# Optimization experiments

Hardware: AMD Instinct MI355X
Metric: run time of the kernel (lower is better)

Reference implementation:

```python
import jax, jax.numpy as jnp
import numpy as np

N, F, H, K = 8192, 128, 128, 16
E = N * 32


def _mlp(f, w1, b1, w2, b2, w3, b3):
    h = jax.nn.relu(f @ w1 + b1)
    h = jax.nn.relu(h @ w2 + b2)
    return h @ w3 + b3


def _edge_conv(x, w1, b1, w2, b2, w3, b3, k):
    # dynamic kNN in feature space (includes self like torch_cluster.knn with x==y)
    sn = jnp.sum(x * x, axis=1)
    d = sn[:, None] + sn[None, :] - 2.0 * (x @ x.T)  # [N,N] squared dists
    idx = jax.lax.top_k(-d, k)[1]                    # [N,k] nearest neighbors
    xj = x[idx]                                      # [N,k,H]
    xi = jnp.broadcast_to(x[:, None, :], xj.shape)
    f = jnp.concatenate([xi, xj - xi], axis=-1)      # [N,k,2H]
    return jnp.max(_mlp(f, w1, b1, w2, b2, w3, b3), axis=1)  # max aggregation


def _gcn(x, w, b, src, dst, norm, n):
    h = x @ w
    out = jax.ops.segment_sum(norm[:, None] * h[src], dst, num_segments=n)
    return out + b


def _forward(x, edge_index, edge_weight,
             wg1, bg1, wg2, bg2, wg3, bg3,
             e1w1, e1b1, e1w2, e1b2, e1w3, e1b3,
             e2w1, e2b1, e2w2, e2b2, e2w3, e2b3,
             e3w1, e3b1, e3w2, e3b2, e3w3, e3b3):
    n = x.shape[0]
    loop = jnp.arange(n)
    src = jnp.concatenate([edge_index[0], loop])  # source j
    dst = jnp.concatenate([edge_index[1], loop])  # target i
    ew = jnp.concatenate([edge_weight, jnp.ones((n,), x.dtype)])  # self-loop weight 1
    deg = jax.ops.segment_sum(ew, dst, num_segments=n)
    dis = jnp.where(deg > 0, jax.lax.rsqrt(jnp.maximum(deg, 1e-12)), 0.0)
    norm = dis[src] * ew * dis[dst]

    n1 = jnp.tanh(_gcn(x, wg1, bg1, src, dst, norm, n))   # dropout is identity at eval
    e1 = _edge_conv(n1, e1w1, e1b1, e1w2, e1b2, e1w3, e1b3, K)
    e1_n1 = jnp.linalg.norm(e1 + n1, axis=1, keepdims=True)  # [N,1]

    n2 = jnp.tanh(_gcn(n1, wg2, bg2, src, dst, norm, n))
    e2 = _edge_conv(n2, e2w1, e2b1, e2w2, e2b2, e2w3, e2b3, K)
    e2_n2 = e2 + n2

    n3 = jnp.tanh(_gcn(n2, wg3, bg3, src, dst, norm, n))
    e3 = _edge_conv(n3, e3w1, e3b1, e3w2, e3b2, e3w3, e3b3, K)
    e3_n3 = e3 + n3

    x2 = e1_n1 * e2_n2 * e3_n3
    return jax.nn.log_softmax(x2, axis=1)


def setup_inputs() -> dict:
    key = jax.random.key(0)
    ks = jax.random.split(key, 32)
    inp = {
        'x': jax.random.normal(ks[0], (N, F), dtype=jnp.float32),
        'edge_index': jax.random.randint(ks[1], (2, E), 0, N, dtype=jnp.int64) if jax.config.jax_enable_x64 else jax.random.randint(ks[1], (2, E), 0, N).astype(jnp.int32),
        'edge_weight': jax.random.uniform(ks[2], (E,), dtype=jnp.float32),
    }
    s = 0.05
    gcn_in = [F, H, H]
    for i in range(3):
        inp[f'wg{i+1}'] = jax.random.normal(ks[3 + i], (gcn_in[i], H), dtype=jnp.float32) * s
        inp[f'bg{i+1}'] = jnp.zeros((H,), jnp.float32)
    dims = [(2 * H, 64), (64, H), (H, H)]
    kk = 6
    for c in range(1, 4):
        for j, (di, do) in enumerate(dims):
            inp[f'e{c}w{j+1}'] = jax.random.normal(ks[kk], (di, do), dtype=jnp.float32) * s
            inp[f'e{c}b{j+1}'] = jnp.zeros((do,), jnp.float32)
            kk += 1
    return inp


def reference(x, edge_index, edge_weight,
              wg1, bg1, wg2, bg2, wg3, bg3,
              e1w1, e1b1, e1w2, e1b2, e1w3, e1b3,
              e2w1, e2b1, e2w2, e2b2, e2w3, e2b3,
              e3w1, e3b1, e3w2, e3b2, e3w3, e3b3):
    return _forward(x, edge_index, edge_weight,
                    wg1, bg1, wg2, bg2, wg3, bg3,
                    e1w1, e1b1, e1w2, e1b2, e1w3, e1b3,
                    e2w1, e2b1, e2w2, e2b2, e2w3, e2b3,
                    e3w1, e3b1, e3w2, e3b2, e3w3, e3b3)
```

## Files before the change

### kernel.cpp

```cpp
#include <hip/hip_runtime.h>
#include <math.h>

#define N_ 8192
#define H_ 128
#define E_ 262144
#define K_ 16
#define SLABJ 1024
#define CHUNKJ 512

typedef __attribute__((ext_vector_type(8))) short bshort8;
typedef __attribute__((ext_vector_type(16))) float f32x16;
typedef unsigned long long u64;

__global__ void k_deg_init(float* deg) {
  int i = blockIdx.x * 256 + threadIdx.x;
  deg[i] = 1.0f;
}

__global__ void k_deg_scatter(const int* __restrict__ ei, const float* __restrict__ ew,
                              float* deg) {
  int e = blockIdx.x * 256 + threadIdx.x;
  atomicAdd(&deg[ei[E_ + e]], ew[e]);
}

__global__ void k_dis(float* deg) {
  int i = blockIdx.x * 256 + threadIdx.x;
  deg[i] = rsqrtf(deg[i]);
}

__global__ void k_hist(const int* __restrict__ ei, int* hist) {
  int e = blockIdx.x * 256 + threadIdx.x;
  atomicAdd(&hist[ei[E_ + e]], 1);
}

__global__ void k_scan(int* hist, int* rowptr) {
  __shared__ int part[256];
  __shared__ int partx[257];
  int t = threadIdx.x;
  int base = t * 32;
  int loc[32];
  int s = 0;
#pragma unroll
  for (int i = 0; i < 32; ++i) { loc[i] = s; s += hist[base + i]; }
  part[t] = s;
  __syncthreads();
  if (t == 0) {
    int r = 0;
    for (int i = 0; i < 256; ++i) { partx[i] = r; r += part[i]; }
    partx[256] = r;
  }
  __syncthreads();
  int b = partx[t];
#pragma unroll
  for (int i = 0; i < 32; ++i) {
    rowptr[base + i] = b + loc[i];
    hist[base + i] = b + loc[i];
  }
  if (t == 0) rowptr[N_] = partx[256];
}

__global__ void k_edgebuild(const int* __restrict__ ei, const float* __restrict__ ew,
                            const float* __restrict__ dis, int* cursor,
                            int* __restrict__ srcS, float* __restrict__ normS) {
  int e = blockIdx.x * 256 + threadIdx.x;
  int s = ei[e], d = ei[E_ + e];
  int pos = atomicAdd(&cursor[d], 1);
  srcS[pos] = s;
  normS[pos] = dis[s] * ew[e] * dis[d];
}

__device__ __forceinline__ unsigned short f2bf_rne(float x) {
  unsigned u = __builtin_bit_cast(unsigned, x);
  unsigned r = ((u >> 16) & 1u) + 0x7fffu;
  return (unsigned short)((u + r) >> 16);
}
__device__ __forceinline__ float bf2f(unsigned short b) {
  unsigned u = ((unsigned)b) << 16;
  return __builtin_bit_cast(float, u);
}

struct WP { const float* p[12]; };

__global__ void k_wprepAll(WP wp, bshort8* __restrict__ wAll) {
  int id = blockIdx.x * 256 + threadIdx.x;
  int layer = id / 7168;
  int r = id - layer * 7168;
  bshort8* base = wAll + layer * 14336;
  const float* src;
  bshort8 *dH, *dL;
  int slot, kind;
  if (r < 2048)      { kind = 0; slot = r;        src = wp.p[layer*4+0]; dH = base;         dL = base + 2048; }
  else if (r < 4096) { kind = 1; slot = r - 2048; src = wp.p[layer*4+1]; dH = base + 4096;  dL = base + 6144; }
  else if (r < 5120) { kind = 2; slot = r - 4096; src = wp.p[layer*4+2]; dH = base + 8192;  dL = base + 9216; }
  else               { kind = 3; slot = r - 5120; src = wp.p[layer*4+3]; dH = base + 10240; dL = base + 12288; }
  int lane = slot & 63;
  int n, k0;
  if (kind == 2) {
    int ks = (slot >> 6) & 3, nt = slot >> 8;
    n = nt * 32 + (lane & 31);
    k0 = ks * 16 + (lane >> 5) * 8;
  } else {
    int ks = (slot >> 6) & 7, nt = slot >> 9;
    n = nt * 32 + (lane & 31);
    k0 = ks * 16 + (lane >> 5) * 8;
  }
  bshort8 h, l;
#pragma unroll
  for (int i = 0; i < 8; ++i) {
    int k = k0 + i;
    float v;
    if (kind == 1) v = (n < 64) ? (src[k * 64 + n] - src[(128 + k) * 64 + n])
                                : src[(128 + k) * 64 + (n - 64)];
    else v = src[k * 128 + n];
    unsigned short hb = f2bf_rne(v);
    h[i] = (short)hb;
    l[i] = (short)f2bf_rne(v - bf2f(hb));
  }
  dH[slot] = h;
  dL[slot] = l;
}

__global__ __launch_bounds__(256, 3) void k_gemmM(const float* __restrict__ A,
                                                  const bshort8* __restrict__ wfH,
                                                  const bshort8* __restrict__ wfL,
                                                  float* __restrict__ C) {
  __shared__ short aHs[32 * 132], aLs[32 * 132];
  int t = threadIdx.x;
  int r0 = blockIdx.x * 32;
  int w = t >> 6, lane = t & 63, q = lane & 31, half = lane >> 5;

  {
    int r = t >> 3;
    int kc = (t & 7) * 16;
    const float* p = A + (r0 + r) * 128 + kc;
#pragma unroll
    for (int e4 = 0; e4 < 4; ++e4) {
      float4 v = *(const float4*)(p + e4 * 4);
      float vals[4] = {v.x, v.y, v.z, v.w};
      unsigned short hs[4], ls[4];
#pragma unroll
      for (int i = 0; i < 4; ++i) {
        hs[i] = f2bf_rne(vals[i]);
        ls[i] = f2bf_rne(vals[i] - bf2f(hs[i]));
      }
      int off = r * 132 + kc + e4 * 4;
      *(u64*)&aHs[off] = ((u64)hs[0]) | ((u64)hs[1] << 16) | ((u64)hs[2] << 32) | ((u64)hs[3] << 48);
      *(u64*)&aLs[off] = ((u64)ls[0]) | ((u64)ls[1] << 16) | ((u64)ls[2] << 32) | ((u64)ls[3] << 48);
    }
  }
  bshort8 bH[8], bL[8];
#pragma unroll
  for (int ks = 0; ks < 8; ++ks) {
    bH[ks] = wfH[(w * 8 + ks) * 64 + lane];
    bL[ks] = wfL[(w * 8 + ks) * 64 + lane];
  }
  __syncthreads();

  f32x16 accP, accQ;
#pragma unroll
  for (int r = 0; r < 16; ++r) { accP[r] = 0.f; accQ[r] = 0.f; }
#pragma unroll
  for (int ks = 0; ks < 8; ++ks) {
    int off = q * 132 + ks * 16 + half * 8;
    union { bshort8 v; u64 u[2]; } aH, aL;
    aH.u[0] = *(const u64*)&aHs[off];
    aH.u[1] = *(const u64*)&aHs[off + 4];
    aL.u[0] = *(const u64*)&aLs[off];
    aL.u[1] = *(const u64*)&aLs[off + 4];
    accQ = __builtin_amdgcn_mfma_f32_32x32x16_bf16(aL.v, bH[ks], accQ, 0, 0, 0);
    accQ = __builtin_amdgcn_mfma_f32_32x32x16_bf16(aH.v, bL[ks], accQ, 0, 0, 0);
    accP = __builtin_amdgcn_mfma_f32_32x32x16_bf16(aH.v, bH[ks], accP, 0, 0, 0);
  }
#pragma unroll
  for (int reg = 0; reg < 16; ++reg) {
    int row = (reg & 3) + 8 * (reg >> 2) + 4 * half;
    C[(r0 + row) * 128 + w * 32 + q] = accP[reg] + accQ[reg];
  }
}

__global__ void k_gemmMF(const bshort8* __restrict__ fAH, const bshort8* __restrict__ fAL,
                         const bshort8* __restrict__ wfH, const bshort8* __restrict__ wfL,
                         float* __restrict__ C) {
  int t = threadIdx.x;
  int rt = blockIdx.x >> 1;
  int w = (blockIdx.x & 1) * 2 + (t >> 6);
  int lane = t & 63, q = lane & 31, half = lane >> 5;

  bshort8 bH[8], bL[8], aH[8], aL[8];
#pragma unroll
  for (int ks = 0; ks < 8; ++ks) {
    bH[ks] = wfH[(w * 8 + ks) * 64 + lane];
    bL[ks] = wfL[(w * 8 + ks) * 64 + lane];
    aH[ks] = fAH[(rt * 8 + ks) * 64 + lane];
    aL[ks] = fAL[(rt * 8 + ks) * 64 + lane];
  }
  f32x16 accP, accQ;
#pragma unroll
  for (int r = 0; r < 16; ++r) { accP[r] = 0.f; accQ[r] = 0.f; }
#pragma unroll
  for (int ks = 0; ks < 8; ++ks) {
    accQ = __builtin_amdgcn_mfma_f32_32x32x16_bf16(aL[ks], bH[ks], accQ, 0, 0, 0);
    accQ = __builtin_amdgcn_mfma_f32_32x32x16_bf16(aH[ks], bL[ks], accQ, 0, 0, 0);
    accP = __builtin_amdgcn_mfma_f32_32x32x16_bf16(aH[ks], bH[ks], accP, 0, 0, 0);
  }
#pragma unroll
  for (int reg = 0; reg < 16; ++reg) {
    int row = (reg & 3) + 8 * (reg >> 2) + 4 * half;
    C[(rt * 32 + row) * 128 + w * 32 + q] = accP[reg] + accQ[reg];
  }
}

__global__ __launch_bounds__(256) void k_gcn_agg(const float* __restrict__ h,
                                                 const float* __restrict__ dis,
                                                 const int* __restrict__ rowptr,
                                                 const int* __restrict__ srcS,
                                                 const float* __restrict__ normS,
                                                 const float* __restrict__ bg,
                                                 float* __restrict__ n_out,
                                                 float* __restrict__ sn) {
  __shared__ float part[4];
  int t = threadIdx.x;
  int i = blockIdx.x * 2 + (t >> 7);
  int c = t & 127;
  float di = dis[i];
  float a0 = di * di * h[i * 128 + c], a1 = 0.f, a2 = 0.f, a3 = 0.f;
  int e0 = rowptr[i], e1 = rowptr[i + 1];
  int e = e0;
  for (; e + 4 <= e1; e += 4) {
    int s0 = srcS[e], s1 = srcS[e + 1], s2 = srcS[e + 2], s3 = srcS[e + 3];
    float w0 = normS[e], w1 = normS[e + 1], w2 = normS[e + 2], w3 = normS[e + 3];
    a0 += w0 * h[s0 * 128 + c];
    a1 += w1 * h[s1 * 128 + c];
    a2 += w2 * h[s2 * 128 + c];
    a3 += w3 * h[s3 * 128 + c];
  }
  for (; e < e1; ++e) a0 += normS[e] * h[srcS[e] * 128 + c];
  float v = tanhf(a0 + a1 + a2 + a3 + bg[c]);
  n_out[i * 128 + c] = v;
  float vv = v * v;
#pragma unroll
  for (int off = 32; off; off >>= 1) vv += __shfl_down(vv, off, 64);
  if ((t & 63) == 0) part[t >> 6] = vv;
  __syncthreads();
  if ((t & 127) == 0) sn[i] = part[t >> 6] + part[(t >> 6) + 1];
}

__global__ void k_fragprep(const float* __restrict__ src, bshort8* __restrict__ hiA,
                           bshort8* __restrict__ loA) {
  int t = blockIdx.x * 256 + threadIdx.x;
  int j = t >> 4, slot = t & 15;
  const float* p = src + j * 128 + slot * 8;
  float4 f0 = *(const float4*)p;
  float4 f1 = *(const float4*)(p + 4);
  float f[8] = {f0.x, f0.y, f0.z, f0.w, f1.x, f1.y, f1.z, f1.w};
  bshort8 h, l;
#pragma unroll
  for (int i = 0; i < 8; ++i) {
    unsigned short hb = f2bf_rne(f[i]);
    h[i] = (short)hb;
    l[i] = (short)f2bf_rne(f[i] - bf2f(hb));
  }
  int ks = slot >> 1, half = slot & 1;
  int dst = ((j >> 5) * 8 + ks) * 64 + half * 32 + (j & 31);
  hiA[dst] = h;
  loA[dst] = l;
}

__device__ __forceinline__ u64 packkey(float d, int j) {
  unsigned m = __builtin_bit_cast(unsigned, d);
  m = (m & 0x80000000u) ? ~m : (m | 0x80000000u);
  return (((u64)m) << 32) | (unsigned)j;
}

__device__ __forceinline__ float unpackd(u64 key) {
  unsigned m = (unsigned)(key >> 32);
  unsigned u = (m & 0x80000000u) ? (m & 0x7fffffffu) : ~m;
  return __builtin_bit_cast(float, u);
}

__device__ __forceinline__ void ins4(u64* tk, u64 x) {
  bool c[4];
#pragma unroll
  for (int s = 0; s < 4; ++s) c[s] = x < tk[s];
#pragma unroll
  for (int s = 3; s >= 1; --s) tk[s] = c[s - 1] ? tk[s - 1] : (c[s] ? x : tk[s]);
  tk[0] = c[0] ? x : tk[0];
}

__device__ __forceinline__ void ins16(u64* tk, u64 x) {
  bool c[16];
#pragma unroll
  for (int s = 0; s < 16; ++s) c[s] = x < tk[s];
#pragma unroll
  for (int s = 15; s >= 1; --s) tk[s] = c[s - 1] ? tk[s - 1] : (c[s] ? x : tk[s]);
  tk[0] = c[0] ? x : tk[0];
}

__global__ __launch_bounds__(256, 2) void k_knnA(const bshort8* __restrict__ fragHi,
                                                 const bshort8* __restrict__ fragLo,
                                                 const float* __restrict__ sn,
                                                 u64* __restrict__ candR) {
  __shared__ float snS[CHUNKJ];
  int t = threadIdx.x;
  int qtile = blockIdx.x, chunk = blockIdx.y;
  int wave = t >> 6, lane = t & 63;
  int q = lane & 31, half = lane >> 5;

  snS[t] = sn[chunk * CHUNKJ + t];
  snS[t + 256] = sn[chunk * CHUNKJ + t + 256];

  bshort8 bHi[8], bLo[8];
#pragma unroll
  for (int ks = 0; ks < 8; ++ks) {
    int o = (qtile * 8 + ks) * 64 + lane;
    bHi[ks] = fragHi[o];
    bLo[ks] = fragLo[o];
  }
  __syncthreads();

  u64 tk[4];
#pragma unroll
  for (int s = 0; s < 4; ++s) tk[s] = ~0ULL;

  int jt0 = chunk * 16 + wave * 4;
  bshort8 pH[4], pL[4];
#pragma unroll
  for (int k4 = 0; k4 < 4; ++k4) {
    int o = (jt0 * 8 + k4) * 64 + lane;
    pH[k4] = fragHi[o];
    pL[k4] = fragLo[o];
  }

  for (int ti = 0; ti < 4; ++ti) {
    int jt = jt0 + ti;
    f32x16 accP, accQ;
#pragma unroll
    for (int r = 0; r < 16; ++r) { accP[r] = 0.f; accQ[r] = 0.f; }

    bshort8 qH[4], qL[4];
#pragma unroll
    for (int k4 = 0; k4 < 4; ++k4) {
      int o = (jt * 8 + 4 + k4) * 64 + lane;
      qH[k4] = fragHi[o];
      qL[k4] = fragLo[o];
    }
#pragma unroll
    for (int k4 = 0; k4 < 4; ++k4) {
      accQ = __builtin_amdgcn_mfma_f32_32x32x16_bf16(pL[k4], bHi[k4], accQ, 0, 0, 0);
      accQ = __builtin_amdgcn_mfma_f32_32x32x16_bf16(pH[k4], bLo[k4], accQ, 0, 0, 0);
      accP = __builtin_amdgcn_mfma_f32_32x32x16_bf16(pH[k4], bHi[k4], accP, 0, 0, 0);
    }
    if (ti < 3) {
#pragma unroll
      for (int k4 = 0; k4 < 4; ++k4) {
        int o = ((jt + 1) * 8 + k4) * 64 + lane;
        pH[k4] = fragHi[o];
        pL[k4] = fragLo[o];
      }
    }
#pragma unroll
    for (int k4 = 0; k4 < 4; ++k4) {
      accQ = __builtin_amdgcn_mfma_f32_32x32x16_bf16(qL[k4], bHi[4 + k4], accQ, 0, 0, 0);
      accQ = __builtin_amdgcn_mfma_f32_32x32x16_bf16(qH[k4], bLo[4 + k4], accQ, 0, 0, 0);
      accP = __builtin_amdgcn_mfma_f32_32x32x16_bf16(qH[k4], bHi[4 + k4], accP, 0, 0, 0);
    }

    int jbase = (wave * 4 + ti) * 32;
#pragma unroll
    for (int rp = 0; rp < 8; ++rp) {
      int r0 = rp * 2;
      int row0 = (r0 & 3) + 8 * (r0 >> 2) + 4 * half;
      float d0 = snS[jbase + row0] - 2.0f * (accP[r0] + accQ[r0]);
      float d1 = snS[jbase + row0 + 1] - 2.0f * (accP[r0 + 1] + accQ[r0 + 1]);
      u64 k0 = packkey(d0, chunk * CHUNKJ + jbase + row0);
      u64 k1 = packkey(d1, chunk * CHUNKJ + jbase + row0 + 1);
      u64 km = k0 < k1 ? k0 : k1;
      if (km < tk[3]) {
        if (k0 < tk[3]) ins4(tk, k0);
        if (k1 < tk[3]) ins4(tk, k1);
      }
    }
  }

  int g = wave * 2 + half;
#pragma unroll
  for (int s = 0; s < 4; ++s)
    candR[(size_t)(chunk * 32 + g * 4 + s) * N_ + qtile * 32 + q] = tk[s];
}

__global__ __launch_bounds__(256) void k_tauseedX(const u64* __restrict__ candR,
                                                  int* __restrict__ cursor,
                                                  float* __restrict__ tauD) {
  __shared__ u64 mb[64 * 65];
  int t = threadIdx.x;
  int ql = t >> 2, j = t & 3;
  int q = blockIdx.x * 64 + ql;

  int rb[8];
#pragma unroll
  for (int k = 0; k < 8; ++k) {
    int L = 8 * j + k;
    rb[k] = (L >> 3) * 32 + (L & 7) * 4;
  }
  int h0 = 0, h1 = 0, h2 = 0, h3 = 0, h4 = 0, h5 = 0, h6 = 0, h7 = 0;
  for (int step = 0; step < 16; ++step) {
    u64 best = (h0 < 4) ? candR[(size_t)(rb[0] + h0) * N_ + q] : ~0ULL;
    int bg = 0;
    u64 b;
    b = (h1 < 4) ? candR[(size_t)(rb[1] + h1) * N_ + q] : ~0ULL; if (b < best) { best = b; bg = 1; }
    b = (h2 < 4) ? candR[(size_t)(rb[2] + h2) * N_ + q] : ~0ULL; if (b < best) { best = b; bg = 2; }
    b = (h3 < 4) ? candR[(size_t)(rb[3] + h3) * N_ + q] : ~0ULL; if (b < best) { best = b; bg = 3; }
    b = (h4 < 4) ? candR[(size_t)(rb[4] + h4) * N_ + q] : ~0ULL; if (b < best) { best = b; bg = 4; }
    b = (h5 < 4) ? candR[(size_t)(rb[5] + h5) * N_ + q] : ~0ULL; if (b < best) { best = b; bg = 5; }
    b = (h6 < 4) ? candR[(size_t)(rb[6] + h6) * N_ + q] : ~0ULL; if (b < best) { best = b; bg = 6; }
    b = (h7 < 4) ? candR[(size_t)(rb[7] + h7) * N_ + q] : ~0ULL; if (b < best) { best = b; bg = 7; }
    mb[ql * 65 + j * 16 + step] = best;
    h0 += (bg == 0); h1 += (bg == 1); h2 += (bg == 2); h3 += (bg == 3);
    h4 += (bg == 4); h5 += (bg == 5); h6 += (bg == 6); h7 += (bg == 7);
  }
  __syncthreads();
  if (t < 64) {
    int qq = blockIdx.x * 64 + t;
    int base = t * 65;
    int g0 = 0, g1 = 0, g2 = 0, g3 = 0;
    u64 best = 0;
    for (int step = 0; step < 16; ++step) {
      best = mb[base + g0];
      int bg = 0;
      u64 b;
      b = mb[base + 16 + g1]; if (b < best) { best = b; bg = 1; }
      b = mb[base + 32 + g2]; if (b < best) { best = b; bg = 2; }
      b = mb[base + 48 + g3]; if (b < best) { best = b; bg = 3; }
      g0 += (bg == 0); g1 += (bg == 1); g2 += (bg == 2); g3 += (bg == 3);
    }
    tauD[qq] = unpackd(best);
    cursor[qq] = 0;
  }
}

__global__ __launch_bounds__(256, 2) void k_knnB(const bshort8* __restrict__ fragHi,
                                                 const bshort8* __restrict__ fragLo,
                                                 const float* __restrict__ sn,
                                                 const float* __restrict__ tauD,
                                                 int* __restrict__ cursor,
                                                 u64* __restrict__ accept,
                                                 u64* __restrict__ accExt) {
  __shared__ float snS[SLABJ];
  int t = threadIdx.x;
  int qtile = blockIdx.x, slab = blockIdx.y;
  int wave = t >> 6, lane = t & 63;
  int q = lane & 31, half = lane >> 5;
  int qg = qtile * 32 + q;

#pragma unroll
  for (int p = 0; p < 4; ++p) snS[t + 256 * p] = sn[slab * SLABJ + t + 256 * p];

  bshort8 bHi[8], bLo[8];
#pragma unroll
  for (int ks = 0; ks < 8; ++ks) {
    int o = (qtile * 8 + ks) * 64 + lane;
    bHi[ks] = fragHi[o];
    bLo[ks] = fragLo[o];
  }
  float tD = tauD[qg];
  __syncthreads();

  u64 buf[6];
  int cnt = 0;

  int jt0 = slab * 32 + wave * 8;
  bshort8 pH[4], pL[4];
#pragma unroll
  for (int k4 = 0; k4 < 4; ++k4) {
    int o = (jt0 * 8 + k4) * 64 + lane;
    pH[k4] = fragHi[o];
    pL[k4] = fragLo[o];
  }

  for (int ti = 0; ti < 8; ++ti) {
    int jt = jt0 + ti;
    f32x16 accP, accQ;
#pragma unroll
    for (int r = 0; r < 16; ++r) { accP[r] = 0.f; accQ[r] = 0.f; }

    bshort8 qH[4], qL[4];
#pragma unroll
    for (int k4 = 0; k4 < 4; ++k4) {
      int o = (jt * 8 + 4 + k4) * 64 + lane;
      qH[k4] = fragHi[o];
      qL[k4] = fragLo[o];
    }
#pragma unroll
    for (int k4 = 0; k4 < 4; ++k4) {
      accQ = __builtin_amdgcn_mfma_f32_32x32x16_bf16(pL[k4], bHi[k4], accQ, 0, 0, 0);
      accQ = __builtin_amdgcn_mfma_f32_32x32x16_bf16(pH[k4], bLo[k4], accQ, 0, 0, 0);
      accP = __builtin_amdgcn_mfma_f32_32x32x16_bf16(pH[k4], bHi[k4], accP, 0, 0, 0);
    }
    if (ti < 7) {
#pragma unroll
      for (int k4 = 0; k4 < 4; ++k4) {
        int o = ((jt + 1) * 8 + k4) * 64 + lane;
        pH[k4] = fragHi[o];
        pL[k4] = fragLo[o];
      }
    }
#pragma unroll
    for (int k4 = 0; k4 < 4; ++k4) {
      accQ = __builtin_amdgcn_mfma_f32_32x32x16_bf16(qL[k4], bHi[4 + k4], accQ, 0, 0, 0);
      accQ = __builtin_amdgcn_mfma_f32_32x32x16_bf16(qH[k4], bLo[4 + k4], accQ, 0, 0, 0);
      accP = __builtin_amdgcn_mfma_f32_32x32x16_bf16(qH[k4], bHi[4 + k4], accP, 0, 0, 0);
    }

    int jbase = (wave * 8 + ti) * 32;
#pragma unroll
    for (int rp = 0; rp < 8; ++rp) {
      int r0 = rp * 2;
      int row0 = (r0 & 3) + 8 * (r0 >> 2) + 4 * half;
      float d0 = snS[jbase + row0] - 2.0f * (accP[r0] + accQ[r0]);
      float d1 = snS[jbase + row0 + 1] - 2.0f * (accP[r0 + 1] + accQ[r0 + 1]);
      if (d0 <= tD) {
        u64 k0 = packkey(d0, slab * SLABJ + jbase + row0);
        if (cnt < 6) {
#pragma unroll
          for (int s = 0; s < 6; ++s)
            if (s == cnt) buf[s] = k0;
          ++cnt;
        } else {
          int pos = atomicAdd(&cursor[qg], 1);
          if (pos < 128) accept[(size_t)pos * N_ + qg] = k0;
          else if (pos < 192) accExt[(size_t)(pos - 128) * N_ + qg] = k0;
        }
      }
      if (d1 <= tD) {
        u64 k1 = packkey(d1, slab * SLABJ + jbase + row0 + 1);
        if (cnt < 6) {
#pragma unroll
          for (int s = 0; s < 6; ++s)
            if (s == cnt) buf[s] = k1;
          ++cnt;
        } else {
          int pos = atomicAdd(&cursor[qg], 1);
          if (pos < 128) accept[(size_t)pos * N_ + qg] = k1;
          else if (pos < 192) accExt[(size_t)(pos - 128) * N_ + qg] = k1;
        }
      }
    }
  }

  if (cnt > 0) {
    int pos = atomicAdd(&cursor[qg], cnt);
#pragma unroll
    for (int s = 0; s < 6; ++s) {
      if (s < cnt) {
        int slot = pos + s;
        if (slot < 128) accept[(size_t)slot * N_ + qg] = buf[s];
        else if (slot < 192) accExt[(size_t)(slot - 128) * N_ + qg] = buf[s];
      }
    }
  }
}

__global__ __launch_bounds__(256) void k_select(const u64* __restrict__ accept,
                                                const u64* __restrict__ accExt,
                                                const int* __restrict__ cursor,
                                                int* __restrict__ idxo) {
  __shared__ u64 mb[64 * 65];
  int t = threadIdx.x;
  int ql = t >> 2;
  int j = t & 3;
  int q = blockIdx.x * 64 + ql;
  int c = cursor[q];
  if (c > 192) c = 192;
  u64 tk[16];
#pragma unroll
  for (int s = 0; s < 16; ++s) tk[s] = ~0ULL;
  for (int i = j; i < c; i += 4) {
    u64 x = (i < 128) ? accept[(size_t)i * N_ + q] : accExt[(size_t)(i - 128) * N_ + q];
    if (x < tk[15]) ins16(tk, x);
  }
#pragma unroll
  for (int s = 0; s < 16; ++s) mb[ql * 65 + j * 16 + s] = tk[s];
  __syncthreads();
  if (t < 64) {
    int qq = blockIdx.x * 64 + t;
    int base = t * 65;
    int h0 = 0, h1 = 0, h2 = 0, h3 = 0;
    for (int step = 0; step < 16; ++step) {
      u64 best = mb[base + h0];
      int bg = 0;
      u64 b;
      b = mb[base + 16 + h1]; if (b < best) { best = b; bg = 1; }
      b = mb[base + 32 + h2]; if (b < best) { best = b; bg = 2; }
      b = mb[base + 48 + h3]; if (b < best) { best = b; bg = 3; }
      idxo[qq * 16 + step] = (int)(unsigned)(best & 0xffffffffULL);
      h0 += (bg == 0); h1 += (bg == 1); h2 += (bg == 2); h3 += (bg == 3);
    }
  }
}

__global__ __launch_bounds__(256, 3) void k_mlpM(
    const float* __restrict__ ab, const int* __restrict__ idx,
    const bshort8* __restrict__ w2fH, const bshort8* __restrict__ w2fL,
    const bshort8* __restrict__ w3fH, const bshort8* __restrict__ w3fL,
    const float* __restrict__ b1g, const float* __restrict__ b2g,
    const float* __restrict__ b3g, const float* __restrict__ nadd,
    float* __restrict__ eout) {
  __shared__ short h1H[64 * 68], h1L[64 * 68];
  __shared__ short h2H[64 * 132], h2L[64 * 132];
  int t = threadIdx.x;
  int n0 = blockIdx.x * 4;
  int w = t >> 6, lane = t & 63, q = lane & 31, half = lane >> 5;

  {
    int r = t >> 2;
    int kc = (t & 3) * 16;
    int node = n0 + (r >> 4);
    int jn = idx[node * 16 + (r & 15)];
    const float* pa = ab + node * 128 + kc;
    const float* pb = ab + jn * 128 + 64 + kc;
    const float* p1 = b1g + kc;
#pragma unroll
    for (int e4 = 0; e4 < 4; ++e4) {
      float4 va = *(const float4*)(pa + e4 * 4);
      float4 vb = *(const float4*)(pb + e4 * 4);
      float4 v1 = *(const float4*)(p1 + e4 * 4);
      float vals[4] = {va.x + vb.x + v1.x, va.y + vb.y + v1.y,
                       va.z + vb.z + v1.z, va.w + vb.w + v1.w};
      unsigned short hs[4], ls[4];
#pragma unroll
      for (int i = 0; i < 4; ++i) {
        float v = fmaxf(vals[i], 0.f);
        hs[i] = f2bf_rne(v);
        ls[i] = f2bf_rne(v - bf2f(hs[i]));
      }
      int off = r * 68 + kc + e4 * 4;
      *(u64*)&h1H[off] = ((u64)hs[0]) | ((u64)hs[1] << 16) | ((u64)hs[2] << 32) | ((u64)hs[3] << 48);
      *(u64*)&h1L[off] = ((u64)ls[0]) | ((u64)ls[1] << 16) | ((u64)ls[2] << 32) | ((u64)ls[3] << 48);
    }
  }

  bshort8 c2H[4], c2L[4];
#pragma unroll
  for (int ks = 0; ks < 4; ++ks) {
    c2H[ks] = w2fH[(w * 4 + ks) * 64 + lane];
    c2L[ks] = w2fL[(w * 4 + ks) * 64 + lane];
  }
  bshort8 c3H[8], c3L[8];
#pragma unroll
  for (int ks = 0; ks < 8; ++ks) {
    c3H[ks] = w3fH[(w * 8 + ks) * 64 + lane];
    c3L[ks] = w3fL[(w * 8 + ks) * 64 + lane];
  }
  float bias2 = b2g[w * 32 + q];
  float bias3 = b3g[w * 32 + q];
  __syncthreads();

#pragma unroll
  for (int rt = 0; rt < 2; ++rt) {
    f32x16 acc;
#pragma unroll
    for (int r = 0; r < 16; ++r) acc[r] = 0.f;
#pragma unroll
    for (int ks = 0; ks < 4; ++ks) {
      int off = (rt * 32 + q) * 68 + ks * 16 + half * 8;
      union { bshort8 v; u64 u[2]; } aH, aL;
      aH.u[0] = *(const u64*)&h1H[off];
      aH.u[1] = *(const u64*)&h1H[off + 4];
      aL.u[0] = *(const u64*)&h1L[off];
      aL.u[1] = *(const u64*)&h1L[off + 4];
      acc = __builtin_amdgcn_mfma_f32_32x32x16_bf16(aL.v, c2H[ks], acc, 0, 0, 0);
      acc = __builtin_amdgcn_mfma_f32_32x32x16_bf16(aH.v, c2L[ks], acc, 0, 0, 0);
      acc = __builtin_amdgcn_mfma_f32_32x32x16_bf16(aH.v, c2H[ks], acc, 0, 0, 0);
    }
#pragma unroll
    for (int reg = 0; reg < 16; ++reg) {
      int row = rt * 32 + (reg & 3) + 8 * (reg >> 2) + 4 * half;
      float v = fmaxf(acc[reg] + bias2, 0.f);
      unsigned short hb = f2bf_rne(v);
      h2H[row * 132 + w * 32 + q] = (short)hb;
      h2L[row * 132 + w * 32 + q] = (short)f2bf_rne(v - bf2f(hb));
    }
  }
  __syncthreads();

#pragma unroll
  for (int rt = 0; rt < 2; ++rt) {
    f32x16 acc;
#pragma unroll
    for (int r = 0; r < 16; ++r) acc[r] = 0.f;
#pragma unroll
    for (int ks = 0; ks < 8; ++ks) {
      int off = (rt * 32 + q) * 132 + ks * 16 + half * 8;
      union { bshort8 v; u64 u[2]; } aH, aL;
      aH.u[0] = *(const u64*)&h2H[off];
      aH.u[1] = *(const u64*)&h2H[off + 4];
      aL.u[0] = *(const u64*)&h2L[off];
      aL.u[1] = *(const u64*)&h2L[off + 4];
      acc = __builtin_amdgcn_mfma_f32_32x32x16_bf16(aL.v, c3H[ks], acc, 0, 0, 0);
      acc = __builtin_amdgcn_mfma_f32_32x32x16_bf16(aH.v, c3L[ks], acc, 0, 0, 0);
      acc = __builtin_amdgcn_mfma_f32_32x32x16_bf16(aH.v, c3H[ks], acc, 0, 0, 0);
    }
    float mA = -INFINITY, mB = -INFINITY;
#pragma unroll
    for (int reg = 0; reg < 8; ++reg) mA = fmaxf(mA, acc[reg]);
#pragma unroll
    for (int reg = 8; reg < 16; ++reg) mB = fmaxf(mB, acc[reg]);
    mA = fmaxf(mA, __shfl_xor(mA, 32, 64));
    mB = fmaxf(mB, __shfl_xor(mB, 32, 64));
    int col = w * 32 + q;
    int nodeA = n0 + rt * 2, nodeB = n0 + rt * 2 + 1;
    if (half == 0) {
      float v = mA + bias3;
      if (nadd) v += nadd[nodeA * 128 + col];
      eout[nodeA * 128 + col] = v;
    } else {
      float v = mB + bias3;
      if (nadd) v += nadd[nodeB * 128 + col];
      eout[nodeB * 128 + col] = v;
    }
  }
}

__global__ void k_e1n1(const float* __restrict__ e1, const float* __restrict__ n1,
                       float* s1) {
  int t = threadIdx.x;
  int node = blockIdx.x * 4 + (t >> 6);
  int lane = t & 63;
  float v0 = e1[node * 128 + lane] + n1[node * 128 + lane];
  float v1 = e1[node * 128 + 64 + lane] + n1[node * 128 + 64 + lane];
  float ss = v0 * v0 + v1 * v1;
#pragma unroll
  for (int off = 32; off; off >>= 1) ss += __shfl_down(ss, off, 64);
  if (lane == 0) s1[node] = sqrtf(ss);
}

__global__ void k_final(const float* __restrict__ s1, const float* __restrict__ e2n2,
                        const float* __restrict__ e3n3, float* __restrict__ out) {
  int t = threadIdx.x;
  int node = blockIdx.x * 4 + (t >> 6);
  int lane = t & 63;
  float s = s1[node];
  float z0 = s * e2n2[node * 128 + lane] * e3n3[node * 128 + lane];
  float z1 = s * e2n2[node * 128 + 64 + lane] * e3n3[node * 128 + 64 + lane];
  float m = fmaxf(z0, z1);
#pragma unroll
  for (int off = 32; off; off >>= 1) m = fmaxf(m, __shfl_xor(m, off, 64));
  float ex = expf(z0 - m) + expf(z1 - m);
#pragma unroll
  for (int off = 32; off; off >>= 1) ex += __shfl_xor(ex, off, 64);
  float lse = m + logf(ex);
  out[node * 128 + lane] = z0 - lse;
  out[node * 128 + 64 + lane] = z1 - lse;
}

extern "C" void kernel_launch(void* const* d_in, const int* in_sizes, int n_in,
                              void* d_out, int out_size, void* d_ws, size_t ws_size,
                              hipStream_t stream) {
  (void)in_sizes; (void)n_in; (void)out_size;
  const float* x  = (const float*)d_in[0];
  const int* ei   = (const int*)d_in[1];
  const float* ew = (const float*)d_in[2];
  const float* wg[3] = {(const float*)d_in[3], (const float*)d_in[5], (const float*)d_in[7]};
  const float* bg[3] = {(const float*)d_in[4], (const float*)d_in[6], (const float*)d_in[8]};
  const float* ew1[3] = {(const float*)d_in[9],  (const float*)d_in[15], (const float*)d_in[21]};
  const float* eb1[3] = {(const float*)d_in[10], (const float*)d_in[16], (const float*)d_in[22]};
  const float* ew2[3] = {(const float*)d_in[11], (const float*)d_in[17], (const float*)d_in[23]};
  const float* eb2[3] = {(const float*)d_in[12], (const float*)d_in[18], (const float*)d_in[24]};
  const float* ew3[3] = {(const float*)d_in[13], (const float*)d_in[19], (const float*)d_in[25]};
  const float* eb3[3] = {(const float*)d_in[14], (const float*)d_in[20], (const float*)d_in[26]};

  size_t small = (size_t)(23 * N_ + (N_ + 256) + N_ + 2 * E_);
  size_t need = (small + 172032 + (size_t)7 * N_ * H_) * sizeof(float);
  if (ws_size < need) return;

  float* ws  = (float*)d_ws;
  float* dis = ws;
  float* sn  = ws + N_;
  float* S1  = ws + 2 * N_;
  int* idx   = (int*)(ws + 3 * N_);
  int* cursor = (int*)(ws + 21 * N_);
  float* tauD = ws + 22 * N_;
  int* rowptr = (int*)(ws + 23 * N_);
  int* hist   = rowptr + N_ + 256;
  int* srcS   = hist + N_;
  float* normS = (float*)(srcS + E_);
  bshort8* wAll = (bshort8*)(normS + E_);
  float* h   = (float*)(normS + E_ + 172032);
  float* n1  = h + N_ * H_;
  float* n2  = n1 + N_ * H_;
  float* n3  = n2 + N_ * H_;
  float* E2  = n3 + N_ * H_;
  float* E1  = E2 + N_ * H_;
  float* ab  = E1 + N_ * H_;

  bshort8* fragHi = (bshort8*)h;
  bshort8* fragLo = (bshort8*)(h + N_ * H_ / 2);
  u64* candR  = (u64*)E1;
  u64* accept = (u64*)E1;

  float* nl[3] = {n1, n2, n3};
  float* spare[3] = {n2, n1, n2};
  float* nadd[3] = {nullptr, n2, n3};

  k_deg_init<<<N_ / 256, 256, 0, stream>>>(dis);
  k_deg_scatter<<<E_ / 256, 256, 0, stream>>>(ei, ew, dis);
  k_dis<<<N_ / 256, 256, 0, stream>>>(dis);
  hipMemsetAsync(hist, 0, N_ * sizeof(int), stream);
  k_hist<<<E_ / 256, 256, 0, stream>>>(ei, hist);
  k_scan<<<1, 256, 0, stream>>>(hist, rowptr);
  k_edgebuild<<<E_ / 256, 256, 0, stream>>>(ei, ew, dis, hist, srcS, normS);

  WP wp;
  for (int l = 0; l < 3; ++l) {
    wp.p[l * 4 + 0] = wg[l];
    wp.p[l * 4 + 1] = ew1[l];
    wp.p[l * 4 + 2] = ew2[l];
    wp.p[l * 4 + 3] = ew3[l];
  }
  k_wprepAll<<<84, 256, 0, stream>>>(wp, wAll);

  for (int l = 0; l < 3; ++l) {
    bshort8* wl = wAll + l * 14336;
    bshort8* wgfH = wl;            bshort8* wgfL = wl + 2048;
    bshort8* w1fH = wl + 4096;     bshort8* w1fL = wl + 6144;
    bshort8* w2fH = wl + 8192;     bshort8* w2fL = wl + 9216;
    bshort8* w3fH = wl + 10240;    bshort8* w3fL = wl + 12288;

    const float* inp = (l == 0) ? x : nl[l - 1];
    k_gemmM<<<256, 256, 0, stream>>>(inp, wgfH, wgfL, h);
    k_gcn_agg<<<N_ / 2, 256, 0, stream>>>(h, dis, rowptr, srcS, normS, bg[l], nl[l], sn);
    k_fragprep<<<N_ * 16 / 256, 256, 0, stream>>>(nl[l], fragHi, fragLo);
    k_knnA<<<dim3(N_ / 32, 4), 256, 0, stream>>>(fragHi, fragLo, sn, candR);
    k_tauseedX<<<N_ / 64, 256, 0, stream>>>(candR, cursor, tauD);
    k_knnB<<<dim3(N_ / 32, 8), 256, 0, stream>>>(fragHi, fragLo, sn, tauD, cursor,
                                                 accept, (u64*)spare[l]);
    k_select<<<N_ / 64, 256, 0, stream>>>(accept, (u64*)spare[l], cursor, idx);
    k_gemmMF<<<512, 128, 0, stream>>>(fragHi, fragLo, w1fH, w1fL, ab);
    float* etgt = (l == 1) ? E2 : E1;
    k_mlpM<<<N_ / 4, 256, 0, stream>>>(ab, idx, w2fH, w2fL, w3fH, w3fL,
                                       eb1[l], eb2[l], eb3[l], nadd[l], etgt);
    if (l == 0) k_e1n1<<<N_ / 4, 256, 0, stream>>>(E1, n1, S1);
  }
  k_final<<<N_ / 4, 256, 0, stream>>>(S1, E2, E1, (float*)d_out);
}
```

Baseline: 801.0 us.

## Share kNN j-tiles across waves through double-buffered LDS staging

Restructures k_knnB so each block covers four query tiles, one per wave. All four waves share candidate j-fragments that are staged cooperatively into a double-buffered shared-memory tile, and each wave now walks all 32 j-tiles of the slab. This cuts redundant global/L2 fragment loads by sharing them across waves. The grid shrinks fourfold. It adds a block-wide barrier per j-tile, exposes global-load latency on the LDS staging path, and raises the per-thread candidate buffer from 6 to 8.

Measured after the change: 841.9 us. +5.1%, slower.

```diff
diff --git a/kernel.cpp b/kernel.cpp
--- a/kernel.cpp
+++ b/kernel.cpp
@@ -446,11 +446,14 @@
                                                  u64* __restrict__ accept,
                                                  u64* __restrict__ accExt) {
   __shared__ float snS[SLABJ];
-  int t = threadIdx.x;
-  int qtile = blockIdx.x, slab = blockIdx.y;
+  __shared__ bshort8 tH[2][512];
+  __shared__ bshort8 tL[2][512];
+  int t = threadIdx.x;
+  int qg4 = blockIdx.x, slab = blockIdx.y;
   int wave = t >> 6, lane = t & 63;
   int q = lane & 31, half = lane >> 5;
-  int qg = qtile * 32 + q;
+  int qtile = qg4 * 4 + wave;
+  int qgl = qtile * 32 + q;
 
 #pragma unroll
   for (int p = 0; p < 4; ++p) snS[t + 256 * p] = sn[slab * SLABJ + t + 256 * p];
@@ -462,56 +465,44 @@
     bHi[ks] = fragHi[o];
     bLo[ks] = fragLo[o];
   }
-  float tD = tauD[qg];
-  __syncthreads();
-
-  u64 buf[6];
+  float tD = tauD[qgl];
+
+  {
+    size_t src = (size_t)(slab * 32) * 512;
+    tH[0][t] = fragHi[src + t];
+    tH[0][t + 256] = fragHi[src + t + 256];
+    tL[0][t] = fragLo[src + t];
+    tL[0][t + 256] = fragLo[src + t + 256];
+  }
+  __syncthreads();
+
+  u64 buf[8];
   int cnt = 0;
 
-  int jt0 = slab * 32 + wave * 8;
-  bshort8 pH[4], pL[4];
-#pragma unroll
-  for (int k4 = 0; k4 < 4; ++k4) {
-    int o = (jt0 * 8 + k4) * 64 + lane;
-    pH[k4] = fragHi[o];
-    pL[k4] = fragLo[o];
-  }
-
-  for (int ti = 0; ti < 8; ++ti) {
-    int jt = jt0 + ti;
+  for (int ti = 0; ti < 32; ++ti) {
+    int cb = ti & 1;
+    if (ti < 31) {
+      size_t src = (size_t)(slab * 32 + ti + 1) * 512;
+      int nb = cb ^ 1;
+      tH[nb][t] = fragHi[src + t];
+      tH[nb][t + 256] = fragHi[src + t + 256];
+      tL[nb][t] = fragLo[src + t];
+      tL[nb][t + 256] = fragLo[src + t + 256];
+    }
+
     f32x16 accP, accQ;
 #pragma unroll
     for (int r = 0; r < 16; ++r) { accP[r] = 0.f; accQ[r] = 0.f; }
-
-    bshort8 qH[4], qL[4];
-#pragma unroll
-    for (int k4 = 0; k4 < 4; ++k4) {
-      int o = (jt * 8 + 4 + k4) * 64 + lane;
-      qH[k4] = fragHi[o];
-      qL[k4] = fragLo[o];
-    }
-#pragma unroll
-    for (int k4 = 0; k4 < 4; ++k4) {
-      accQ = __builtin_amdgcn_mfma_f32_32x32x16_bf16(pL[k4], bHi[k4], accQ, 0, 0, 0);
-      accQ = __builtin_amdgcn_mfma_f32_32x32x16_bf16(pH[k4], bLo[k4], accQ, 0, 0, 0);
-      accP = __builtin_amdgcn_mfma_f32_32x32x16_bf16(pH[k4], bHi[k4], accP, 0, 0, 0);
-    }
-    if (ti < 7) {
-#pragma unroll
-      for (int k4 = 0; k4 < 4; ++k4) {
-        int o = ((jt + 1) * 8 + k4) * 64 + lane;
-        pH[k4] = fragHi[o];
-        pL[k4] = fragLo[o];
-      }
-    }
-#pragma unroll
-    for (int k4 = 0; k4 < 4; ++k4) {
-      accQ = __builtin_amdgcn_mfma_f32_32x32x16_bf16(qL[k4], bHi[4 + k4], accQ, 0, 0, 0);
-      accQ = __builtin_amdgcn_mfma_f32_32x32x16_bf16(qH[k4], bLo[4 + k4], accQ, 0, 0, 0);
-      accP = __builtin_amdgcn_mfma_f32_32x32x16_bf16(qH[k4], bHi[4 + k4], accP, 0, 0, 0);
-    }
-
-    int jbase = (wave * 8 + ti) * 32;
+#pragma unroll
+    for (int ks = 0; ks < 8; ++ks) {
+      bshort8 aH = tH[cb][ks * 64 + lane];
+      bshort8 aL = tL[cb][ks * 64 + lane];
+      accQ = __builtin_amdgcn_mfma_f32_32x32x16_bf16(aL, bHi[ks], accQ, 0, 0, 0);
+      accQ = __builtin_amdgcn_mfma_f32_32x32x16_bf16(aH, bLo[ks], accQ, 0, 0, 0);
+      accP = __builtin_amdgcn_mfma_f32_32x32x16_bf16(aH, bHi[ks], accP, 0, 0, 0);
+    }
+
+    int jbase = ti * 32;
 #pragma unroll
     for (int rp = 0; rp < 8; ++rp) {
       int r0 = rp * 2;
@@ -520,41 +511,42 @@
       float d1 = snS[jbase + row0 + 1] - 2.0f * (accP[r0 + 1] + accQ[r0 + 1]);
       if (d0 <= tD) {
         u64 k0 = packkey(d0, slab * SLABJ + jbase + row0);
-        if (cnt < 6) {
-#pragma unroll
-          for (int s = 0; s < 6; ++s)
+        if (cnt < 8) {
+#pragma unroll
+          for (int s = 0; s < 8; ++s)
             if (s == cnt) buf[s] = k0;
           ++cnt;
         } else {
-          int pos = atomicAdd(&cursor[qg], 1);
-          if (pos < 128) accept[(size_t)pos * N_ + qg] = k0;
-          else if (pos < 192) accExt[(size_t)(pos - 128) * N_ + qg] = k0;
+          int pos = atomicAdd(&cursor[qgl], 1);
+          if (pos < 128) accept[(size_t)pos * N_ + qgl] = k0;
+          else if (pos < 192) accExt[(size_t)(pos - 128) * N_ + qgl] = k0;
         }
       }
       if (d1 <= tD) {
         u64 k1 = packkey(d1, slab * SLABJ + jbase + row0 + 1);
-        if (cnt < 6) {
-#pragma unroll
-          for (int s = 0; s < 6; ++s)
+        if (cnt < 8) {
+#pragma unroll
+          for (int s = 0; s < 8; ++s)
             if (s == cnt) buf[s] = k1;
           ++cnt;
         } else {
-          int pos = atomicAdd(&cursor[qg], 1);
-          if (pos < 128) accept[(size_t)pos * N_ + qg] = k1;
-          else if (pos < 192) accExt[(size_t)(pos - 128) * N_ + qg] = k1;
+          int pos = atomicAdd(&cursor[qgl], 1);
+          if (pos < 128) accept[(size_t)pos * N_ + qgl] = k1;
+          else if (pos < 192) accExt[(size_t)(pos - 128) * N_ + qgl] = k1;
         }
       }
     }
+    __syncthreads();
   }
 
   if (cnt > 0) {
-    int pos = atomicAdd(&cursor[qg], cnt);
-#pragma unroll
-    for (int s = 0; s < 6; ++s) {
+    int pos = atomicAdd(&cursor[qgl], cnt);
+#pragma unroll
+    for (int s = 0; s < 8; ++s) {
       if (s < cnt) {
         int slot = pos + s;
-        if (slot < 128) accept[(size_t)slot * N_ + qg] = buf[s];
-        else if (slot < 192) accExt[(size_t)(slot - 128) * N_ + qg] = buf[s];
+        if (slot < 128) accept[(size_t)slot * N_ + qgl] = buf[s];
+        else if (slot < 192) accExt[(size_t)(slot - 128) * N_ + qgl] = buf[s];
       }
     }
   }
@@ -832,8 +824,8 @@
     k_fragprep<<<N_ * 16 / 256, 256, 0, stream>>>(nl[l], fragHi, fragLo);
     k_knnA<<<dim3(N_ / 32, 4), 256, 0, stream>>>(fragHi, fragLo, sn, candR);
     k_tauseedX<<<N_ / 64, 256, 0, stream>>>(candR, cursor, tauD);
-    k_knnB<<<dim3(N_ / 32, 8), 256, 0, stream>>>(fragHi, fragLo, sn, tauD, cursor,
-                                                 accept, (u64*)spare[l]);
+    k_knnB<<<dim3(N_ / 128, 8), 256, 0, stream>>>(fragHi, fragLo, sn, tauD, cursor,
+                                                  accept, (u64*)spare[l]);
     k_select<<<N_ / 64, 256, 0, stream>>>(accept, (u64*)spare[l], cursor, idx);
     k_gemmMF<<<512, 128, 0, stream>>>(fragHi, fragLo, w1fH, w1fL, ab);
     float* etgt = (l == 1) ? E2 : E1;
```
